# Kernel optimization log

Measured on AMD Instinct MI355X. Metric: run time of the kernel, lower is better.

The kernel has to match this reference:

```python
import jax, jax.numpy as jnp
import numpy as np

B = 131072
N = 19  # num_features, fixed by the hard-coded 19x19 correlation matrix


def _make_corr():
    corr = np.eye(N, dtype=np.float32)
    for i, j, v in [(0, 1, 0.9088), (2, 3, 0.7964), (2, 4, 0.6972),
                    (2, 9, -0.6945), (4, 9, -0.6679)]:
        corr[i, j] = corr[j, i] = v
    return jnp.asarray(corr)


def setup_inputs() -> dict:
    key = jax.random.key(0)
    ks = jax.random.split(key, 9)
    bound = 1.0 / np.sqrt(N)  # torch nn.Linear default init range

    def linear_params(k):
        kw, kb = jax.random.split(k)
        W = jax.random.uniform(kw, (N, N), jnp.float32, -bound, bound)
        b = jax.random.uniform(kb, (N,), jnp.float32, -bound, bound)
        return W, b

    Wq, bq = linear_params(ks[0])
    Wk, bk = linear_params(ks[1])
    Wv, bv = linear_params(ks[2])
    Wo, bo = linear_params(ks[3])
    features = jax.random.normal(ks[4], (B, N), jnp.float32)
    return {
        "features": features,
        "Wq": Wq, "bq": bq,
        "Wk": Wk, "bk": bk,
        "Wv": Wv, "bv": bv,
        "Wo": Wo, "bo": bo,
        "corr": _make_corr(),
        "temperature": jnp.array(1.0, jnp.float32),
    }


def reference(features, Wq, bq, Wk, bk, Wv, bv, Wo, bo, corr, temperature):
    # Projections (torch Linear: x @ W.T + b)
    Q = features @ Wq.T + bq  # [B, N]
    K = features @ Wk.T + bk  # [B, N]
    V = features @ Wv.T + bv  # [B, N]

    # Outer-product scores: bmm(Q[:, :, None], K[:, None, :]) -> [B, N, N]
    scores = Q[:, :, None] * K[:, None, :]

    # correlation_weight = (corr @ K.T).T = K @ corr.T ; mean over features -> [B]
    cw_mean = (K @ corr.T).mean(axis=-1)
    scores = scores * cw_mean[:, None, None]

    attention = jax.nn.softmax(scores / temperature, axis=-1)  # [B, N, N]

    # Elementwise combine (attention * V broadcast over the query axis)
    attended = attention * V[:, None, :]  # [B, N, N]

    output = attended @ Wo.T + bo  # [B, N, N]

    # Residual: features broadcast over the query axis
    return features[:, None, :] + output  # [B, N, N]
```

## Files before the change

kernel.cpp:

```cpp
#include <hip/hip_runtime.h>

#define B_TOTAL 131072
#define N 19
#define BB 13
#define ROWS (BB * N)
#define NPAD 20
#define OUT_PER_G (BB * N * N)
#define NBLOCKS ((B_TOTAL + BB - 1) / BB)

typedef __attribute__((ext_vector_type(16))) float sfloat16;
typedef __attribute__((ext_vector_type(2)))  float sfloat2;

__global__ void __launch_bounds__(256, 5) cga_kernel(
    const float* __restrict__ feats,
    const float* __restrict__ Wq, const float* __restrict__ bq,
    const float* __restrict__ Wk, const float* __restrict__ bk,
    const float* __restrict__ Wv, const float* __restrict__ bv,
    const float* __restrict__ Wo, const float* __restrict__ bo,
    const float* __restrict__ corr,
    const float* __restrict__ temp,
    float* __restrict__ out)
{
    __shared__ __align__(16) float feat_s[BB * NPAD];
    __shared__ __align__(16) float k_s[BB * NPAD];
    __shared__ __align__(16) float v_s[BB * NPAD];
    __shared__ __align__(16) float c_s[NPAD];
    __shared__ __align__(16) float bo_s[NPAD];
    __shared__ __align__(16) float wq_s[N * NPAD];
    __shared__ __align__(16) float wk_s[N * NPAD];
    __shared__ __align__(16) float wv_s[N * NPAD];
    __shared__ __align__(16) float out_s[OUT_PER_G];

    const int t  = threadIdx.x;
    const int b0 = blockIdx.x * BB;
    const int bl = t / N;
    const int i  = t - bl * N;
    const bool active = (t < ROWS);

    if (active) {
        int gidx = b0 * N + t;
        feat_s[bl * NPAD + i] = (gidx < B_TOTAL * N) ? feats[gidx] : 0.f;
    }
    {
        int idx = t;
        int r = idx / N, c = idx - r * N;
        wq_s[r * NPAD + c] = Wq[idx];
        wk_s[r * NPAD + c] = Wk[idx];
        wv_s[r * NPAD + c] = Wv[idx];
        idx = t + 256;
        if (idx < N * N) {
            r = idx / N; c = idx - r * N;
            wq_s[r * NPAD + c] = Wq[idx];
            wk_s[r * NPAD + c] = Wk[idx];
            wv_s[r * NPAD + c] = Wv[idx];
        }
    }
    if (t < N) {
        float s = 0.f;
#pragma unroll
        for (int r = 0; r < N; ++r) s += corr[r * N + t];
        c_s[t]  = s * (1.0f / N);
        bo_s[t] = bo[t];
    }
    const float invT = 1.0f / temp[0];
    __syncthreads();

    float q_i = 0.f, k_i = 0.f, v_i = 0.f;
    if (active) {
        float f[NPAD];
        const float4* fp = (const float4*)(&feat_s[bl * NPAD]);
#pragma unroll
        for (int c4 = 0; c4 < 5; ++c4) {
            float4 x = fp[c4];
            f[c4*4+0] = x.x; f[c4*4+1] = x.y; f[c4*4+2] = x.z; f[c4*4+3] = x.w;
        }
        q_i = bq[i]; k_i = bk[i]; v_i = bv[i];
        const float4* wq4 = (const float4*)(&wq_s[i * NPAD]);
        const float4* wk4 = (const float4*)(&wk_s[i * NPAD]);
        const float4* wv4 = (const float4*)(&wv_s[i * NPAD]);
#pragma unroll
        for (int c4 = 0; c4 < 5; ++c4) {
            const int j0 = 4 * c4;
            float4 aq = wq4[c4], ak = wk4[c4], av = wv4[c4];
            q_i = fmaf(f[j0+0], aq.x, q_i);
            k_i = fmaf(f[j0+0], ak.x, k_i);
            v_i = fmaf(f[j0+0], av.x, v_i);
            q_i = fmaf(f[j0+1], aq.y, q_i);
            k_i = fmaf(f[j0+1], ak.y, k_i);
            v_i = fmaf(f[j0+1], av.y, v_i);
            q_i = fmaf(f[j0+2], aq.z, q_i);
            k_i = fmaf(f[j0+2], ak.z, k_i);
            v_i = fmaf(f[j0+2], av.z, v_i);
            if (j0 + 3 < N) {
                q_i = fmaf(f[j0+3], aq.w, q_i);
                k_i = fmaf(f[j0+3], ak.w, k_i);
                v_i = fmaf(f[j0+3], av.w, v_i);
            }
        }
        k_s[bl * NPAD + i] = k_i;
        v_s[bl * NPAD + i] = v_i;
    }
    __syncthreads();

    if (active) {
        float K[NPAD], V[NPAD];
        const float4* kp = (const float4*)(&k_s[bl * NPAD]);
        const float4* vp = (const float4*)(&v_s[bl * NPAD]);
#pragma unroll
        for (int c4 = 0; c4 < 5; ++c4) {
            float4 x = kp[c4];
            K[c4*4+0] = x.x; K[c4*4+1] = x.y; K[c4*4+2] = x.z; K[c4*4+3] = x.w;
            float4 y = vp[c4];
            V[c4*4+0] = y.x; V[c4*4+1] = y.y; V[c4*4+2] = y.z; V[c4*4+3] = y.w;
        }
        float cw = 0.f;
#pragma unroll
        for (int j = 0; j < N; ++j) cw = fmaf(c_s[j], K[j], cw);
        const float a = q_i * cw * invT;

        float m = -1e30f;
#pragma unroll
        for (int j = 0; j < N; ++j) m = fmaxf(m, a * K[j]);
        float z = 0.f;
        float p[N];
#pragma unroll
        for (int j = 0; j < N; ++j) {
            float e = __expf(fmaf(a, K[j], -m));
            p[j] = e * V[j];
            z += e;
        }
        const float invZ = 1.0f / z;

        const int obase = t * N;
        const int fbase = bl * NPAD;
#pragma unroll
        for (int k = 0; k < N; ++k) {
            sfloat16 w0; sfloat2 w1; float w2;
            asm volatile(
                "s_load_dwordx16 %0, %3, %4\n\t"
                "s_load_dwordx2  %1, %3, %5\n\t"
                "s_load_dword    %2, %3, %6\n\t"
                "s_waitcnt lgkmcnt(0)"
                : "=s"(w0), "=s"(w1), "=s"(w2)
                : "s"(Wo), "i"(k * 76), "i"(k * 76 + 64), "i"(k * 76 + 72));
            float acc = 0.f;
#pragma unroll
            for (int j = 0; j < 16; ++j) acc = fmaf(p[j], w0[j], acc);
            acc = fmaf(p[16], w1[0], acc);
            acc = fmaf(p[17], w1[1], acc);
            acc = fmaf(p[18], w2,    acc);
            out_s[obase + k] = feat_s[fbase + k] + bo_s[k] + acc * invZ;
        }
    }
    __syncthreads();

    const int outbase = b0 * (N * N);
#pragma unroll
    for (int r = 0; r < (OUT_PER_G + 255) / 256; ++r) {
        int idx = r * 256 + t;
        int go  = outbase + idx;
        if (idx < OUT_PER_G && go < B_TOTAL * N * N)
            out[go] = out_s[idx];
    }
}

extern "C" void kernel_launch(void* const* d_in, const int* in_sizes, int n_in,
                              void* d_out, int out_size, void* d_ws, size_t ws_size,
                              hipStream_t stream) {
    const float* feats = (const float*)d_in[0];
    const float* Wq    = (const float*)d_in[1];
    const float* bq    = (const float*)d_in[2];
    const float* Wk    = (const float*)d_in[3];
    const float* bk    = (const float*)d_in[4];
    const float* Wv    = (const float*)d_in[5];
    const float* bv    = (const float*)d_in[6];
    const float* Wo    = (const float*)d_in[7];
    const float* bo    = (const float*)d_in[8];
    const float* corr  = (const float*)d_in[9];
    const float* temp  = (const float*)d_in[10];
    float* out = (float*)d_out;

    cga_kernel<<<NBLOCKS, 256, 0, stream>>>(feats, Wq, bq, Wk, bk, Wv, bv,
                                            Wo, bo, corr, temp, out);
}
```

Before: 250.9 us.

## Use 16 batches per 320-thread block with float4 output stores

Raises the batch count per block from 13 to 16 and the block size from 256 to 320 threads, so each block's output tile (16*361 floats) divides by 4 and can be written with aligned float4 stores. Because the batch size divides evenly, the bounds checks on loads and stores are removed. The inline-asm scalar loads of Wo are replaced by plain indexed loads, and the compiler is left to schedule them. The larger LDS footprint and higher thread count may lower occupancy, and the compiler may not keep Wo in scalar registers.

```diff
diff --git a/kernel.cpp b/kernel.cpp
--- a/kernel.cpp
+++ b/kernel.cpp
@@ -2,16 +2,14 @@
 
 #define B_TOTAL 131072
 #define N 19
-#define BB 13
+#define BB 16
 #define ROWS (BB * N)
+#define NT 320
 #define NPAD 20
 #define OUT_PER_G (BB * N * N)
-#define NBLOCKS ((B_TOTAL + BB - 1) / BB)
+#define NBLOCKS (B_TOTAL / BB)
 
-typedef __attribute__((ext_vector_type(16))) float sfloat16;
-typedef __attribute__((ext_vector_type(2)))  float sfloat2;
-
-__global__ void __launch_bounds__(256, 5) cga_kernel(
+__global__ void __launch_bounds__(NT, 5) cga_kernel(
     const float* __restrict__ feats,
     const float* __restrict__ Wq, const float* __restrict__ bq,
     const float* __restrict__ Wk, const float* __restrict__ bk,
@@ -38,8 +36,7 @@
     const bool active = (t < ROWS);
 
     if (active) {
-        int gidx = b0 * N + t;
-        feat_s[bl * NPAD + i] = (gidx < B_TOTAL * N) ? feats[gidx] : 0.f;
+        feat_s[bl * NPAD + i] = feats[b0 * N + t];
     }
     {
         int idx = t;
@@ -47,7 +44,7 @@
         wq_s[r * NPAD + c] = Wq[idx];
         wk_s[r * NPAD + c] = Wk[idx];
         wv_s[r * NPAD + c] = Wv[idx];
-        idx = t + 256;
+        idx = t + NT;
         if (idx < N * N) {
             r = idx / N; c = idx - r * N;
             wq_s[r * NPAD + c] = Wq[idx];
@@ -135,32 +132,22 @@
         const int fbase = bl * NPAD;
 #pragma unroll
         for (int k = 0; k < N; ++k) {
-            sfloat16 w0; sfloat2 w1; float w2;
-            asm volatile(
-                "s_load_dwordx16 %0, %3, %4\n\t"
-                "s_load_dwordx2  %1, %3, %5\n\t"
-                "s_load_dword    %2, %3, %6\n\t"
-                "s_waitcnt lgkmcnt(0)"
-                : "=s"(w0), "=s"(w1), "=s"(w2)
-                : "s"(Wo), "i"(k * 76), "i"(k * 76 + 64), "i"(k * 76 + 72));
             float acc = 0.f;
 #pragma unroll
-            for (int j = 0; j < 16; ++j) acc = fmaf(p[j], w0[j], acc);
-            acc = fmaf(p[16], w1[0], acc);
-            acc = fmaf(p[17], w1[1], acc);
-            acc = fmaf(p[18], w2,    acc);
+            for (int j = 0; j < N; ++j) acc = fmaf(p[j], Wo[k * N + j], acc);
             out_s[obase + k] = feat_s[fbase + k] + bo_s[k] + acc * invZ;
         }
     }
     __syncthreads();
 
-    const int outbase = b0 * (N * N);
+    {
+        const float4* src = (const float4*)out_s;
+        float4* dst = (float4*)(out + (size_t)blockIdx.x * OUT_PER_G);
 #pragma unroll
-    for (int r = 0; r < (OUT_PER_G + 255) / 256; ++r) {
-        int idx = r * 256 + t;
-        int go  = outbase + idx;
-        if (idx < OUT_PER_G && go < B_TOTAL * N * N)
-            out[go] = out_s[idx];
+        for (int r = 0; r < (OUT_PER_G / 4 + NT - 1) / NT; ++r) {
+            int idx = r * NT + t;
+            if (idx < OUT_PER_G / 4) dst[idx] = src[idx];
+        }
     }
 }
 
@@ -180,6 +167,6 @@
     const float* temp  = (const float*)d_in[10];
     float* out = (float*)d_out;
 
-    cga_kernel<<<NBLOCKS, 256, 0, stream>>>(feats, Wq, bq, Wk, bk, Wv, bv,
-                                            Wo, bo, corr, temp, out);
+    cga_kernel<<<NBLOCKS, NT, 0, stream>>>(feats, Wq, bq, Wk, bk, Wv, bv,
+                                           Wo, bo, corr, temp, out);
 }
```

After: 247.8 us. Within noise of the previous version (-1.2%).
